# Kernel tuning notes

Measured on AMD Instinct MI355X. Metric: run time of the kernel, lower is better.

The kernel has to match this reference:

```python
import jax, jax.numpy as jnp
import numpy as np

B, D = 8192, 1024
TEMPERATURE = 0.05
NEG_INF = -9e15


def setup_inputs() -> dict:
    key = jax.random.key(0)
    k1, k2, k3 = jax.random.split(key, 3)
    emb = jax.random.normal(k1, (B, D), dtype=jnp.float32)
    # L2-normalize so sim/temperature is numerically sane (as in real usage)
    emb = emb / jnp.linalg.norm(emb, axis=-1, keepdims=True)
    relations = jax.random.randint(k2, (B,), 0, 128, dtype=jnp.int64)
    is_true_samples = jax.random.bernoulli(k3, 0.5, (B,))
    return {"embeddings": emb, "relations": relations, "is_true_samples": is_true_samples}


def reference(embeddings, relations, is_true_samples):
    b = embeddings.shape[0]
    # [B, B] similarity, diagonal masked to -9e15 as in the original
    sim = jnp.matmul(embeddings, embeddings.T) / TEMPERATURE
    eye = jnp.eye(b, dtype=bool)
    sim = jnp.where(eye, NEG_INF, sim)
    # positive_pairs[i, j] = is_true[i] & is_true[j] & (rel[i] == rel[j]) & (i != j)
    pos = (
        (relations[:, None] == relations[None, :])
        & is_true_samples[:, None]
        & is_true_samples[None, :]
        & ~eye
    )
    exp_sim = jnp.exp(sim)                      # diagonal exp(-9e15) -> 0
    sum_exp = exp_sim.sum(axis=1)               # [B]
    numer = jnp.where(pos, exp_sim, 0.0).sum(axis=1)  # [B]
    has_pos = pos.any(axis=1)                   # [B]
    numer_safe = jnp.where(has_pos, numer, 1.0)
    losses = -jnp.log(numer_safe / (sum_exp + 1e-8))
    n_rows = has_pos.sum()
    loss = jnp.where(
        n_rows > 0,
        jnp.where(has_pos, losses, 0.0).sum() / jnp.maximum(n_rows, 1).astype(losses.dtype),
        jnp.asarray(0.0, dtype=losses.dtype),
    )
    num_positives = n_rows  # rows having at least one positive, as in the original
    return loss, num_positives
```

## Files before the change

### kernel.cpp

```cpp
#include <hip/hip_runtime.h>
#include <hip/hip_bf16.h>
#include <hip/hip_fp8.h>
#include <stdint.h>

#define NB 8192
#define ND 1024
#define SCALE 20.0f
#define PRESCALE 16.0f
#define EXPSCALE (SCALE / (PRESCALE * PRESCALE))

typedef __bf16 bf16x8 __attribute__((ext_vector_type(8)));
typedef float  f32x4  __attribute__((ext_vector_type(4)));

__device__ inline void detect_formats(const void* rel_raw, const void* ist_raw,
                                      int& rel64, int& bmode) {
  const unsigned int* r = (const unsigned int*)rel_raw;
  int is64 = 1;
  for (int i = 1; i < 256; i += 2) {
    if (r[i] != 0u) { is64 = 0; break; }
  }
  rel64 = is64;
  const unsigned int* t = (const unsigned int*)ist_raw;
  bool sawf = false, sawbig = false;
  for (int i = 0; i < 64; ++i) {
    unsigned int w = t[i];
    if (w == 0x3F800000u) sawf = true;
    else if (w > 1u) sawbig = true;
  }
  bmode = sawf ? 2 : (sawbig ? 1 : 0);
}

__device__ inline int decode_key(const void* rel_raw, const void* ist_raw,
                                 int rel64, int bmode, int i) {
  const int* r32 = (const int*)rel_raw;
  int r = rel64 ? r32[2 * i] : r32[i];
  int truth;
  if (bmode == 1)      truth = (((const unsigned char*)ist_raw)[i] != 0);
  else if (bmode == 2) truth = (((const float*)ist_raw)[i] != 0.0f);
  else                 truth = (((const int*)ist_raw)[i] != 0);
  return truth ? r : -1;
}

__device__ inline bf16x8 cvt8(const float4& a, const float4& b) {
  bf16x8 v;
  v[0] = (__bf16)a.x; v[1] = (__bf16)a.y; v[2] = (__bf16)a.z; v[3] = (__bf16)a.w;
  v[4] = (__bf16)b.x; v[5] = (__bf16)b.y; v[6] = (__bf16)b.z; v[7] = (__bf16)b.w;
  return v;
}

__device__ inline unsigned long long cvt8f8(const float4& a, const float4& b) {
  float v[8] = {a.x, a.y, a.z, a.w, b.x, b.y, b.z, b.w};
  unsigned long long pk = 0;
#pragma unroll
  for (int i = 0; i < 8; ++i) {
    __hip_fp8_e4m3 h(v[i] * PRESCALE);
    pk |= (unsigned long long)(unsigned char)h.__x << (8 * i);
  }
  return pk;
}

__global__ void prep_kernel(const float* __restrict__ emb,
                            const void* __restrict__ rel_raw,
                            const void* __restrict__ ist_raw,
                            unsigned char* __restrict__ emb8,
                            float* __restrict__ sum_exp,
                            float* __restrict__ numer,
                            int* __restrict__ key) {
  int tid = blockIdx.x * 256 + threadIdx.x;
  size_t base = (size_t)tid * 8;
  if (base < (size_t)NB * ND) {
    float4 a = *(const float4*)(emb + base);
    float4 b = *(const float4*)(emb + base + 4);
    *(unsigned long long*)(emb8 + base) = cvt8f8(a, b);
  }
  if (tid < NB) { sum_exp[tid] = 0.f; numer[tid] = 0.f; }
  __shared__ int s_rel64, s_bmode;
  if (blockIdx.x < 32) {
    if (threadIdx.x == 0) {
      int a, b; detect_formats(rel_raw, ist_raw, a, b);
      s_rel64 = a; s_bmode = b;
    }
    __syncthreads();
    int i = blockIdx.x * 256 + threadIdx.x;
    key[i] = decode_key(rel_raw, ist_raw, s_rel64, s_bmode, i);
  }
}

__global__ void prep_small_kernel(const void* __restrict__ rel_raw,
                                  const void* __restrict__ ist_raw,
                                  float* __restrict__ sum_exp,
                                  float* __restrict__ numer,
                                  int* __restrict__ key) {
  int i = blockIdx.x * 256 + threadIdx.x;
  sum_exp[i] = 0.f; numer[i] = 0.f;
  __shared__ int s_rel64, s_bmode;
  if (threadIdx.x == 0) {
    int a, b; detect_formats(rel_raw, ist_raw, a, b);
    s_rel64 = a; s_bmode = b;
  }
  __syncthreads();
  key[i] = decode_key(rel_raw, ist_raw, s_rel64, s_bmode, i);
}


__global__ __launch_bounds__(256, 4)
void gemm_f8w_kernel(const unsigned char* __restrict__ emb8,
                     const int* __restrict__ key,
                     float* __restrict__ sum_exp,
                     float* __restrict__ numer) {
  __shared__ unsigned char sT[3][2][8192];
  __shared__ int keyR[128], keyC[128];

  const int bid = blockIdx.x;
  const int t = (bid & 7) * 260 + (bid >> 3);
  int r = (int)((sqrtf(8.f * (float)t + 1.f) - 1.f) * 0.5f);
  while ((r + 1) * (r + 2) / 2 <= t) ++r;
  while (r * (r + 1) / 2 > t) --r;
  const int bx = r, by = t - r * (r + 1) / 2;
  const bool diag = (bx == by);
  const int rowBase = by * 128, colBase = bx * 128;

  const int tid = threadIdx.x;
  const int wid = tid >> 6;
  const int l   = tid & 63;
  const int wr  = wid >> 1;
  const int wc  = wid & 1;

  const int row = l & 15;
  const int ks  = l >> 4;
  const int X   = ((row >> 1) & 3) << 1;
  const int rd0 = row * 64 + ((ks) ^ X) * 8;
  const int rd1 = row * 64 + ((4 + ks) ^ X) * 8;

  const int srow = l >> 2;
  const int Xs   = ((srow >> 1) & 3) << 1;
  const int scol = ((2 * (l & 3)) ^ Xs) * 8;

  if (tid < 128) keyR[tid] = key[rowBase + tid];
  else           keyC[tid - 128] = key[colBase + tid - 128];
  asm volatile("" ::: "memory");

  const size_t aOff0 = (size_t)(rowBase + (wid * 2 + 0) * 16 + srow) * ND + scol;
  const size_t aOff1 = (size_t)(rowBase + (wid * 2 + 1) * 16 + srow) * ND + scol;
  const size_t bOff0 = (size_t)(colBase + (wid * 2 + 0) * 16 + srow) * ND + scol;
  const size_t bOff1 = (size_t)(colBase + (wid * 2 + 1) * 16 + srow) * ND + scol;
  const int dst0 = (wid * 2 + 0) * 1024 + l * 16;
  const int dst1 = (wid * 2 + 1) * 1024 + l * 16;

#define STAGE(buf, k0)                                                         \
  do {                                                                         \
    __builtin_amdgcn_global_load_lds(                                          \
        (const __attribute__((address_space(1))) void*)(emb8 + aOff0 + (k0)),  \
        (__attribute__((address_space(3))) void*)&sT[buf][0][dst0], 16, 0, 0); \
    __builtin_amdgcn_global_load_lds(                                          \
        (const __attribute__((address_space(1))) void*)(emb8 + aOff1 + (k0)),  \
        (__attribute__((address_space(3))) void*)&sT[buf][0][dst1], 16, 0, 0); \
    __builtin_amdgcn_global_load_lds(                                          \
        (const __attribute__((address_space(1))) void*)(emb8 + bOff0 + (k0)),  \
        (__attribute__((address_space(3))) void*)&sT[buf][1][dst0], 16, 0, 0); \
    __builtin_amdgcn_global_load_lds(                                          \
        (const __attribute__((address_space(1))) void*)(emb8 + bOff1 + (k0)),  \
        (__attribute__((address_space(3))) void*)&sT[buf][1][dst1], 16, 0, 0); \
  } while (0)

  STAGE(0, 0);

  f32x4 acc[4][4] = {};
  int rb = 0, wb = 1;

#pragma unroll 1
  for (int kt = 0; kt < 16; ++kt) {
    if (kt < 15) {
      STAGE(wb, (kt + 1) * 64);
      asm volatile("s_waitcnt vmcnt(4) lgkmcnt(0)" ::: "memory");
    } else {
      asm volatile("s_waitcnt vmcnt(0) lgkmcnt(0)" ::: "memory");
    }
    __builtin_amdgcn_s_barrier();
    asm volatile("" ::: "memory");

    const unsigned char* cA = &sT[rb][0][0];
    const unsigned char* cB = &sT[rb][1][0];
    long af[4], bfr[4];
#pragma unroll
    for (int m = 0; m < 4; ++m)
      af[m] = *(const long*)&cA[(wr * 4 + m) * 1024 + rd0];
#pragma unroll
    for (int n = 0; n < 4; ++n)
      bfr[n] = *(const long*)&cB[(wc * 4 + n) * 1024 + rd0];
    __builtin_amdgcn_s_setprio(1);
#pragma unroll
    for (int m = 0; m < 4; ++m)
#pragma unroll
      for (int n = 0; n < 4; ++n)
        acc[m][n] = __builtin_amdgcn_mfma_f32_16x16x32_fp8_fp8(af[m], bfr[n], acc[m][n], 0, 0, 0);
    __builtin_amdgcn_s_setprio(0);
#pragma unroll
    for (int m = 0; m < 4; ++m)
      af[m] = *(const long*)&cA[(wr * 4 + m) * 1024 + rd1];
#pragma unroll
    for (int n = 0; n < 4; ++n)
      bfr[n] = *(const long*)&cB[(wc * 4 + n) * 1024 + rd1];
    __builtin_amdgcn_s_setprio(1);
#pragma unroll
    for (int m = 0; m < 4; ++m)
#pragma unroll
      for (int n = 0; n < 4; ++n)
        acc[m][n] = __builtin_amdgcn_mfma_f32_16x16x32_fp8_fp8(af[m], bfr[n], acc[m][n], 0, 0, 0);
    __builtin_amdgcn_s_setprio(0);

    rb = (rb == 2) ? 0 : rb + 1;
    wb = (wb == 2) ? 0 : wb + 1;
  }
#undef STAGE

  float cse[4] = {0.f, 0.f, 0.f, 0.f};
  float cnu[4] = {0.f, 0.f, 0.f, 0.f};
#pragma unroll
  for (int m = 0; m < 4; ++m) {
#pragma unroll
    for (int r4 = 0; r4 < 4; ++r4) {
      int li = wr * 64 + m * 16 + (l >> 4) * 4 + r4;
      int gi = rowBase + li;
      int krow = keyR[li];
      float se = 0.f, nu = 0.f;
#pragma unroll
      for (int n = 0; n < 4; ++n) {
        int lj = wc * 64 + n * 16 + (l & 15);
        int gj = colBase + lj;
        float e = __expf(acc[m][n][r4] * EXPSCALE);
        if (gi == gj) e = 0.f;
        bool match = (krow >= 0) && (krow == keyC[lj]);
        se += e;
        if (match) nu += e;
        if (!diag) {
          cse[n] += e;
          if (match) cnu[n] += e;
        }
      }
#pragma unroll
      for (int off = 8; off; off >>= 1) {
        se += __shfl_xor(se, off, 16);
        nu += __shfl_xor(nu, off, 16);
      }
      if ((l & 15) == 0) {
        atomicAdd(&sum_exp[gi], se);
        if (nu != 0.f) atomicAdd(&numer[gi], nu);
      }
    }
  }
  if (!diag) {
#pragma unroll
    for (int n = 0; n < 4; ++n) {
      cse[n] += __shfl_xor(cse[n], 16);
      cse[n] += __shfl_xor(cse[n], 32);
      cnu[n] += __shfl_xor(cnu[n], 16);
      cnu[n] += __shfl_xor(cnu[n], 32);
    }
    if (l < 16) {
#pragma unroll
      for (int n = 0; n < 4; ++n) {
        int gj = colBase + wc * 64 + n * 16 + l;
        atomicAdd(&sum_exp[gj], cse[n]);
        if (cnu[n] != 0.f) atomicAdd(&numer[gj], cnu[n]);
      }
    }
  }
}

__global__ __launch_bounds__(256, 4)
void gemm_fused_f32_kernel(const float* __restrict__ embF,
                           const int* __restrict__ key,
                           float* __restrict__ sum_exp,
                           float* __restrict__ numer) {
  __shared__ __bf16 sA[128 * 64];
  __shared__ __bf16 sB[128 * 64];
  __shared__ int keyR[128], keyC[128];

  const int t = blockIdx.x;
  int r = (int)((sqrtf(8.f * (float)t + 1.f) - 1.f) * 0.5f);
  while ((r + 1) * (r + 2) / 2 <= t) ++r;
  while (r * (r + 1) / 2 > t) --r;
  const int bx = r;
  const int by = t - r * (r + 1) / 2;
  const bool diag = (bx == by);

  const int tid = threadIdx.x;
  const int wid = tid >> 6;
  const int l   = tid & 63;
  const int wr  = wid >> 1;
  const int wc  = wid & 1;
  const int rowBase = by * 128;
  const int colBase = bx * 128;

  if (tid < 128) keyR[tid] = key[rowBase + tid];
  else           keyC[tid - 128] = key[colBase + tid - 128];

  f32x4 acc[4][4] = {};

  for (int k0 = 0; k0 < ND; k0 += 64) {
    __syncthreads();
#pragma unroll
    for (int c = 0; c < 4; ++c) {
      int chunk = tid + c * 256;
      int row = chunk >> 3;
      int ko  = (chunk & 7) * 8;
      const float* gfa = embF + (size_t)(rowBase + row) * ND + k0 + ko;
      const float* gfb = embF + (size_t)(colBase + row) * ND + k0 + ko;
      float4 a0 = *(const float4*)gfa;
      float4 a1 = *(const float4*)(gfa + 4);
      float4 b0 = *(const float4*)gfb;
      float4 b1 = *(const float4*)(gfb + 4);
      *(bf16x8*)&sA[row * 64 + ko] = cvt8(a0, a1);
      *(bf16x8*)&sB[row * 64 + ko] = cvt8(b0, b1);
    }
    __syncthreads();

#pragma unroll
    for (int kk = 0; kk < 2; ++kk) {
      bf16x8 af[4], bfr[4];
#pragma unroll
      for (int m = 0; m < 4; ++m)
        af[m] = *(const bf16x8*)&sA[(wr * 64 + m * 16 + (l & 15)) * 64 + kk * 32 + (l >> 4) * 8];
#pragma unroll
      for (int n = 0; n < 4; ++n)
        bfr[n] = *(const bf16x8*)&sB[(wc * 64 + n * 16 + (l & 15)) * 64 + kk * 32 + (l >> 4) * 8];
#pragma unroll
      for (int m = 0; m < 4; ++m)
#pragma unroll
        for (int n = 0; n < 4; ++n)
          acc[m][n] = __builtin_amdgcn_mfma_f32_16x16x32_bf16(af[m], bfr[n], acc[m][n], 0, 0, 0);
    }
  }

  float cse[4] = {0.f, 0.f, 0.f, 0.f};
  float cnu[4] = {0.f, 0.f, 0.f, 0.f};
#pragma unroll
  for (int m = 0; m < 4; ++m) {
#pragma unroll
    for (int r4 = 0; r4 < 4; ++r4) {
      int li = wr * 64 + m * 16 + (l >> 4) * 4 + r4;
      int gi = rowBase + li;
      int krow = keyR[li];
      float se = 0.f, nu = 0.f;
#pragma unroll
      for (int n = 0; n < 4; ++n) {
        int lj = wc * 64 + n * 16 + (l & 15);
        int gj = colBase + lj;
        float e = __expf(acc[m][n][r4] * SCALE);
        if (gi == gj) e = 0.f;
        bool match = (krow >= 0) && (krow == keyC[lj]);
        se += e;
        if (match) nu += e;
        if (!diag) {
          cse[n] += e;
          if (match) cnu[n] += e;
        }
      }
#pragma unroll
      for (int off = 8; off; off >>= 1) {
        se += __shfl_xor(se, off, 16);
        nu += __shfl_xor(nu, off, 16);
      }
      if ((l & 15) == 0) {
        atomicAdd(&sum_exp[gi], se);
        if (nu != 0.f) atomicAdd(&numer[gi], nu);
      }
    }
  }
  if (!diag) {
#pragma unroll
    for (int n = 0; n < 4; ++n) {
      cse[n] += __shfl_xor(cse[n], 16);
      cse[n] += __shfl_xor(cse[n], 32);
      cnu[n] += __shfl_xor(cnu[n], 16);
      cnu[n] += __shfl_xor(cnu[n], 32);
    }
    if (l < 16) {
#pragma unroll
      for (int n = 0; n < 4; ++n) {
        int gj = colBase + wc * 64 + n * 16 + l;
        atomicAdd(&sum_exp[gj], cse[n]);
        if (cnu[n] != 0.f) atomicAdd(&numer[gj], cnu[n]);
      }
    }
  }
}

__global__ void finalize_kernel(const float* __restrict__ sum_exp,
                                const float* __restrict__ numer,
                                const int* __restrict__ key,
                                float* __restrict__ out) {
  __shared__ int cnt[128];
  __shared__ float wsum[16];
  __shared__ int wcnt[16];
  int tid = threadIdx.x;
  if (tid < 128) cnt[tid] = 0;
  __syncthreads();
  for (int i = tid; i < NB; i += 1024) {
    int k = key[i];
    if (k >= 0) atomicAdd(&cnt[k], 1);
  }
  __syncthreads();
  float ls = 0.f; int np = 0;
  for (int i = tid; i < NB; i += 1024) {
    int k = key[i];
    if (k >= 0 && cnt[k] >= 2) {
      np++;
      ls += logf(sum_exp[i] + 1e-8f) - logf(numer[i]);
    }
  }
  for (int off = 32; off; off >>= 1) {
    ls += __shfl_down(ls, off, 64);
    np += __shfl_down(np, off, 64);
  }
  int w = tid >> 6;
  if ((tid & 63) == 0) { wsum[w] = ls; wcnt[w] = np; }
  __syncthreads();
  if (tid == 0) {
    float s = 0.f; int n = 0;
    for (int i = 0; i < 16; ++i) { s += wsum[i]; n += wcnt[i]; }
    out[0] = (n > 0) ? (s / (float)n) : 0.f;
    out[1] = (float)n;
  }
}

#define NT128 64
#define NTRI128 (NT128 * (NT128 + 1) / 2)

extern "C" void kernel_launch(void* const* d_in, const int* in_sizes, int n_in,
                              void* d_out, int out_size, void* d_ws, size_t ws_size,
                              hipStream_t stream) {
  const float* emb = (const float*)d_in[0];
  const void* rel  = d_in[1];
  const void* ist  = d_in[2];
  float* out = (float*)d_out;

  const size_t emb8Bytes = (size_t)NB * ND;
  const size_t smallBytes = (size_t)NB * 4 * 3;

  char* ws = (char*)d_ws;
  if (ws_size >= emb8Bytes + smallBytes) {
    unsigned char* emb8 = (unsigned char*)ws;
    float* sum_exp = (float*)(ws + emb8Bytes);
    float* numer   = sum_exp + NB;
    int*   key     = (int*)(numer + NB);
    prep_kernel<<<4096, 256, 0, stream>>>(emb, rel, ist, emb8, sum_exp, numer, key);
    gemm_f8w_kernel<<<NTRI128, 256, 0, stream>>>(emb8, key, sum_exp, numer);
    finalize_kernel<<<1, 1024, 0, stream>>>(sum_exp, numer, key, out);
  } else {
    float* sum_exp = (float*)ws;
    float* numer   = sum_exp + NB;
    int*   key     = (int*)(numer + NB);
    prep_small_kernel<<<32, 256, 0, stream>>>(rel, ist, sum_exp, numer, key);
    gemm_fused_f32_kernel<<<NTRI128, 256, 0, stream>>>(emb, key, sum_exp, numer);
    finalize_kernel<<<1, 1024, 0, stream>>>(sum_exp, numer, key, out);
  }
}
```

Baseline: 103.2 us.

## Interleave fp8 K-chunks in global layout to allow 128-bit LDS fragment reads

The prep kernel now writes fp8 embeddings with 8-byte K-chunks permuted inside each 64-byte block, so the two k-slices each lane needs sit next to each other. The GEMM then reads both A and B fragments with a single 16-byte LDS load per tile instead of two 8-byte loads, and drops the XOR swizzle. The goal is to halve LDS read instructions and merge the two MFMA phases under one priority window. Removing the swizzle may bring back LDS bank conflicts on the wider reads.

```diff
diff --git a/kernel.cpp b/kernel.cpp
--- a/kernel.cpp
+++ b/kernel.cpp
@@ -11,6 +11,7 @@
 
 typedef __bf16 bf16x8 __attribute__((ext_vector_type(8)));
 typedef float  f32x4  __attribute__((ext_vector_type(4)));
+typedef long   lx2    __attribute__((ext_vector_type(2)));
 
 __device__ inline void detect_formats(const void* rel_raw, const void* ist_raw,
                                       int& rel64, int& bmode) {
@@ -71,7 +72,9 @@
   if (base < (size_t)NB * ND) {
     float4 a = *(const float4*)(emb + base);
     float4 b = *(const float4*)(emb + base + 4);
-    *(unsigned long long*)(emb8 + base) = cvt8f8(a, b);
+    int u = (int)((base >> 3) & 7);
+    size_t dest = (base & ~(size_t)63) | ((size_t)(2 * (u & 3) + (u >> 2)) << 3);
+    *(unsigned long long*)(emb8 + dest) = cvt8f8(a, b);
   }
   if (tid < NB) { sum_exp[tid] = 0.f; numer[tid] = 0.f; }
   __shared__ int s_rel64, s_bmode;
@@ -104,7 +107,7 @@
 
 
 __global__ __launch_bounds__(256, 4)
-void gemm_f8w_kernel(const unsigned char* __restrict__ emb8,
+void gemm_f8v_kernel(const unsigned char* __restrict__ emb8,
                      const int* __restrict__ key,
                      float* __restrict__ sum_exp,
                      float* __restrict__ numer) {
@@ -126,15 +129,9 @@
   const int wr  = wid >> 1;
   const int wc  = wid & 1;
 
-  const int row = l & 15;
-  const int ks  = l >> 4;
-  const int X   = ((row >> 1) & 3) << 1;
-  const int rd0 = row * 64 + ((ks) ^ X) * 8;
-  const int rd1 = row * 64 + ((4 + ks) ^ X) * 8;
-
+  const int fragOff = (l & 15) * 64 + (l >> 4) * 16;
   const int srow = l >> 2;
-  const int Xs   = ((srow >> 1) & 3) << 1;
-  const int scol = ((2 * (l & 3)) ^ Xs) * 8;
+  const int scol = (l & 3) * 16;
 
   if (tid < 128) keyR[tid] = key[rowBase + tid];
   else           keyC[tid - 128] = key[colBase + tid - 128];
@@ -181,32 +178,24 @@
 
     const unsigned char* cA = &sT[rb][0][0];
     const unsigned char* cB = &sT[rb][1][0];
-    long af[4], bfr[4];
+    lx2 a2[4], b2[4];
 #pragma unroll
     for (int m = 0; m < 4; ++m)
-      af[m] = *(const long*)&cA[(wr * 4 + m) * 1024 + rd0];
+      a2[m] = *(const lx2*)&cA[(wr * 4 + m) * 1024 + fragOff];
 #pragma unroll
     for (int n = 0; n < 4; ++n)
-      bfr[n] = *(const long*)&cB[(wc * 4 + n) * 1024 + rd0];
+      b2[n] = *(const lx2*)&cB[(wc * 4 + n) * 1024 + fragOff];
     __builtin_amdgcn_s_setprio(1);
 #pragma unroll
     for (int m = 0; m < 4; ++m)
 #pragma unroll
       for (int n = 0; n < 4; ++n)
-        acc[m][n] = __builtin_amdgcn_mfma_f32_16x16x32_fp8_fp8(af[m], bfr[n], acc[m][n], 0, 0, 0);
-    __builtin_amdgcn_s_setprio(0);
+        acc[m][n] = __builtin_amdgcn_mfma_f32_16x16x32_fp8_fp8(a2[m][0], b2[n][0], acc[m][n], 0, 0, 0);
 #pragma unroll
     for (int m = 0; m < 4; ++m)
-      af[m] = *(const long*)&cA[(wr * 4 + m) * 1024 + rd1];
-#pragma unroll
-    for (int n = 0; n < 4; ++n)
-      bfr[n] = *(const long*)&cB[(wc * 4 + n) * 1024 + rd1];
-    __builtin_amdgcn_s_setprio(1);
-#pragma unroll
-    for (int m = 0; m < 4; ++m)
 #pragma unroll
       for (int n = 0; n < 4; ++n)
-        acc[m][n] = __builtin_amdgcn_mfma_f32_16x16x32_fp8_fp8(af[m], bfr[n], acc[m][n], 0, 0, 0);
+        acc[m][n] = __builtin_amdgcn_mfma_f32_16x16x32_fp8_fp8(a2[m][1], b2[n][1], acc[m][n], 0, 0, 0);
     __builtin_amdgcn_s_setprio(0);
 
     rb = (rb == 2) ? 0 : rb + 1;
@@ -446,7 +435,7 @@
     float* numer   = sum_exp + NB;
     int*   key     = (int*)(numer + NB);
     prep_kernel<<<4096, 256, 0, stream>>>(emb, rel, ist, emb8, sum_exp, numer, key);
-    gemm_f8w_kernel<<<NTRI128, 256, 0, stream>>>(emb8, key, sum_exp, numer);
+    gemm_f8v_kernel<<<NTRI128, 256, 0, stream>>>(emb8, key, sum_exp, numer);
     finalize_kernel<<<1, 1024, 0, stream>>>(sum_exp, numer, key, out);
   } else {
     float* sum_exp = (float*)ws;
```

After: 100.9 us. 1.02x faster.
